# Kernel tuning notes

Measured on AMD Instinct MI355X. Metric: run time of the kernel, lower is better.

The kernel has to match this reference:

```python
import jax, jax.numpy as jnp
import numpy as np

NMS_THRESH = 0.5
SCORE_THRESH = 0.05
MAX_DET = 300


def _iou_one_vs_all(box, boxes):
    # box: [4] (x1,y1,x2,y2); boxes: [N,4]
    x1 = jnp.maximum(box[0], boxes[:, 0])
    y1 = jnp.maximum(box[1], boxes[:, 1])
    x2 = jnp.minimum(box[2], boxes[:, 2])
    y2 = jnp.minimum(box[3], boxes[:, 3])
    inter = jnp.maximum(x2 - x1, 0.0) * jnp.maximum(y2 - y1, 0.0)
    area_a = (box[2] - box[0]) * (box[3] - box[1])
    area_b = (boxes[:, 2] - boxes[:, 0]) * (boxes[:, 3] - boxes[:, 1])
    union = area_a + area_b - inter
    return inter / jnp.maximum(union, 1e-8)


def _nms_single_class(boxes, scores):
    # Greedy NMS with max_output_size=MAX_DET, matching tf.image.non_max_suppression
    # after score-threshold prefiltering. boxes:[N,4], scores:[N].
    s0 = jnp.where(scores > SCORE_THRESH, scores, -jnp.inf)

    def step(s, _):
        i = jnp.argmax(s)
        si = s[i]
        sel = jnp.isfinite(si)  # False once no candidates remain
        iou = _iou_one_vs_all(boxes[i], boxes)
        s = jnp.where(sel & (iou > NMS_THRESH), -jnp.inf, s)
        s = s.at[i].set(-jnp.inf)
        return s, (i, si, sel)

    _, (idx, sv, sel) = jax.lax.scan(step, s0, None, length=MAX_DET)
    # unselected slots carry -inf score
    return idx.astype(jnp.int32), jnp.where(sel, sv, -jnp.inf)


def _filter_one_image(boxes, classification, other):
    # boxes:[N,4], classification:[N,C], other:[N,D]
    C = classification.shape[1]
    # class-specific NMS (class_specific_filter=True, nms=True)
    idx, sv = jax.vmap(lambda c: _nms_single_class(boxes, classification[:, c]))(
        jnp.arange(C))  # each [C, MAX_DET]
    labels = jnp.broadcast_to(jnp.arange(C)[:, None], idx.shape)
    cand_scores = sv.reshape(-1)          # [C*MAX_DET]
    cand_idx = idx.reshape(-1)
    cand_lab = labels.reshape(-1)
    # global top-k over all per-class survivors
    top_s, top_i = jax.lax.top_k(cand_scores, MAX_DET)
    sel_idx = cand_idx[top_i]
    sel_lab = cand_lab[top_i]
    valid = jnp.isfinite(top_s)
    # pad invalid slots with -1 (matches tf.pad(..., constant_values=-1))
    out_boxes = jnp.where(valid[:, None], boxes[sel_idx], -1.0)
    out_scores = jnp.where(valid, top_s, -1.0)
    out_labels = jnp.where(valid, sel_lab, -1).astype(jnp.int32)
    out_other = jnp.where(valid[:, None], other[sel_idx], -1.0)
    return out_boxes, out_scores, out_labels, out_other


def setup_inputs() -> dict:
    key = jax.random.key(0)
    k1, k2, k3, k4 = jax.random.split(key, 4)
    B, N, C, D = 16, 50000, 8, 2
    xy = jax.random.uniform(k1, (B, N, 2), jnp.float32, 0.0, 512.0)
    wh = jax.random.uniform(k2, (B, N, 2), jnp.float32, 4.0, 100.0)
    boxes = jnp.concatenate([xy, xy + wh], axis=-1)  # valid (x1,y1,x2,y2)
    classification = jax.random.uniform(k3, (B, N, C), jnp.float32)
    other = jax.random.normal(k4, (B, N, D), jnp.float32)
    return {"boxes": boxes, "classification": classification, "other": other}


def reference(boxes, classification, other):
    # tf.map_fn over batch -> vmap over batch
    return jax.vmap(_filter_one_image)(boxes, classification, other)
```

## Files before the change

### kernel.cpp

```cpp
#include <hip/hip_runtime.h>
#include <math.h>
#include <stdint.h>

#define NB 16
#define NN 50000
#define NC 8
#define ND 2
#define MAX_DET 300
#define NMS_T 0.5f
#define SCORE_T 0.05f
#define CAP 1024
#define CUTBIN 252
#define LBUF 128
#define NTILE32 32
#define CHUNK 128
#define NT 512
#define NPI (NN * NC)
#define F4PB (NPI / 4 / NTILE32)

typedef unsigned long long u64;

__device__ __forceinline__ float neg_inf() { return -__builtin_inff(); }

__device__ __forceinline__ bool iou_gt(float ax1, float ay1, float ax2, float ay2,
                                       float area_a,
                                       float bx1, float by1, float bx2, float by2) {
    float x1 = fmaxf(ax1, bx1), y1 = fmaxf(ay1, by1);
    float x2 = fminf(ax2, bx2), y2 = fminf(ay2, by2);
    float inter = __fmul_rn(fmaxf(__fsub_rn(x2, x1), 0.0f),
                            fmaxf(__fsub_rn(y2, y1), 0.0f));
    float area_b = __fmul_rn(__fsub_rn(bx2, bx1), __fsub_rn(by2, by1));
    float uni = __fsub_rn(__fadd_rn(area_a, area_b), inter);
    return inter > __fmul_rn(0.5f, fmaxf(uni, 1e-8f));
}

__device__ __forceinline__ u64 score_key(float s, int n) {
    unsigned u = __float_as_uint(s);
    u ^= (u & 0x80000000u) ? 0xFFFFFFFFu : 0x80000000u;
    return ((u64)u << 32) | (unsigned)(~(unsigned)n);
}

__device__ __forceinline__ u64 shfl_xor_u64(u64 v, int m) {
    unsigned lo = (unsigned)v, hi = (unsigned)(v >> 32);
    lo = __shfl_xor(lo, m, 64);
    hi = __shfl_xor(hi, m, 64);
    return ((u64)hi << 32) | lo;
}

__global__ __launch_bounds__(1024) void compact_kernel(
    const float* __restrict__ cls, int* __restrict__ tcnt_g,
    u64* __restrict__ cand)
{
    const int b = blockIdx.x >> 5, t32 = blockIdx.x & 31;
    const int tid = threadIdx.x;
    __shared__ u64 buf[8][LBUF];
    __shared__ int lcnt[8];
    if (tid < 8) lcnt[tid] = 0;
    __syncthreads();

    const float4* c4 = (const float4*)(cls + (size_t)b * NPI);
    const int f0 = t32 * F4PB, fend = f0 + F4PB;

    for (int f = f0 + tid; f < fend; f += 1024) {
        float4 v = c4[f];
        int cb = (f & 1) * 4;
        int n = f >> 1;
        float vv[4] = {v.x, v.y, v.z, v.w};
        #pragma unroll
        for (int k = 0; k < 4; ++k) {
            float s = vv[k];
            if (s > SCORE_T) {
                int bn = (int)(s * 256.0f); if (bn > 255) bn = 255;
                if (bn >= CUTBIN) {
                    int c = cb + k;
                    int pos = atomicAdd(&lcnt[c], 1);
                    if (pos < LBUF) buf[c][pos] = score_key(s, n);
                }
            }
        }
    }
    __syncthreads();
    {
        int c = tid >> 7, i = tid & (LBUF - 1);
        int m = lcnt[c];
        if (i < (m < LBUF ? m : LBUF))
            cand[(size_t)(((b * 8 + c) * NTILE32) + t32) * LBUF + i] = buf[c][i];
        if (i == 0) tcnt_g[(b * 8 + c) * NTILE32 + t32] = m;
    }
}

__global__ __launch_bounds__(NT) void nms_fused(
    const float* __restrict__ boxes, const float* __restrict__ cls,
    const u64* __restrict__ cand, const int* __restrict__ tcnt_g,
    int* __restrict__ sel_idx, float* __restrict__ sel_score)
{
    const int bc = blockIdx.x;
    const int b = bc >> 3, c = bc & 7;
    const int tid = threadIdx.x;
    const int lane = tid & 63, widx = tid >> 6;
    const float4* bx4 = (const float4*)(boxes + (size_t)b * NN * 4);
    const float* sr = cls + (size_t)b * NN * NC + c;
    int* si = sel_idx + bc * MAX_DET;
    float* ss = sel_score + bc * MAX_DET;

    __shared__ u64 keys[CAP];
    __shared__ int tcnt_s[NTILE32], toff_s[NTILE32];
    __shared__ int sh_total, sh_ovf;
    __shared__ float4 cbox2[2][CHUNK];
    __shared__ float  carea2[2][CHUNK];
    __shared__ int    cidx2[2][CHUNK];
    __shared__ float  cscore2[2][CHUNK];
    __shared__ unsigned M32[4][CHUNK];
    __shared__ unsigned presup4[4][CHUNK];
    __shared__ u64 accmask_s[2];
    __shared__ float4 abox[MAX_DET];
    __shared__ float aarea[MAX_DET];
    __shared__ unsigned bm[(NN + 31) / 32];
    __shared__ float rv[NT];
    __shared__ int   ri[NT];
    __shared__ float sboxsh[5];

    if (tid < 64) {
        int v = (lane < NTILE32) ? tcnt_g[bc * NTILE32 + lane] : 0;
        int incl = v;
        #pragma unroll
        for (int d = 1; d < 32; d <<= 1) {
            int o = __shfl_up(incl, d, 64);
            if (lane >= d) incl += o;
        }
        if (lane < NTILE32) { tcnt_s[lane] = v; toff_s[lane] = incl - v; }
        u64 ov = __ballot(lane < NTILE32 && v > LBUF);
        if (lane == 31) { sh_total = incl; sh_ovf = (ov != 0); }
    }
    __syncthreads();
    const int cnt = sh_total;
    const bool full_fb = sh_ovf || (cnt > CAP);
    const int inSet = cnt < CAP ? cnt : CAP;

    int n_acc = 0;
    if (!full_fb) {
        for (int i = tid; i < CAP; i += NT) keys[i] = 0ull;
        __syncthreads();
        for (int s = tid; s < NTILE32 * LBUF; s += NT) {
            int t = s >> 7, i = s & (LBUF - 1);
            if (i < tcnt_s[t])
                keys[toff_s[t] + i] = cand[(size_t)(bc * NTILE32 + t) * LBUF + i];
        }
        __syncthreads();

        const int p0 = widx * 128 + lane, p1 = p0 + 64;
        u64 v0 = keys[p0];
        u64 v1 = keys[p1];
        #pragma unroll
        for (int k = 2; k <= 128; k <<= 1) {
            #pragma unroll
            for (int j = k >> 1; j > 0; j >>= 1) {
                if (j == 64) {
                    bool dir = ((p0 & k) == 0);
                    if ((v0 < v1) == dir) { u64 t = v0; v0 = v1; v1 = t; }
                } else {
                    bool lower = ((lane & j) == 0);
                    bool dir0 = ((p0 & k) == 0);
                    bool dir1 = ((p1 & k) == 0);
                    u64 o0 = shfl_xor_u64(v0, j);
                    u64 mx0 = v0 > o0 ? v0 : o0, mn0 = v0 > o0 ? o0 : v0;
                    v0 = (lower == dir0) ? mx0 : mn0;
                    u64 o1 = shfl_xor_u64(v1, j);
                    u64 mx1 = v1 > o1 ? v1 : o1, mn1 = v1 > o1 ? o1 : v1;
                    v1 = (lower == dir1) ? mx1 : mn1;
                }
            }
        }
        __syncthreads();
        for (int k = 256; k <= CAP; k <<= 1) {
            keys[p0] = v0; keys[p1] = v1;
            __syncthreads();
            for (int j = k >> 1; j >= 128; j >>= 1) {
                int p = tid;
                int i = 2 * p - (p & (j - 1));
                int ix = i + j;
                bool dir = ((i & k) == 0);
                u64 a = keys[i], b2 = keys[ix];
                if ((a < b2) == dir) { keys[i] = b2; keys[ix] = a; }
                __syncthreads();
            }
            v0 = keys[p0]; v1 = keys[p1];
            {
                bool dir = ((p0 & k) == 0);
                if ((v0 < v1) == dir) { u64 t = v0; v0 = v1; v1 = t; }
            }
            #pragma unroll
            for (int j = 32; j > 0; j >>= 1) {
                bool lower = ((lane & j) == 0);
                bool dir = ((p0 & k) == 0);
                u64 o0 = shfl_xor_u64(v0, j);
                u64 mx0 = v0 > o0 ? v0 : o0, mn0 = v0 > o0 ? o0 : v0;
                v0 = (lower == dir) ? mx0 : mn0;
                u64 o1 = shfl_xor_u64(v1, j);
                u64 mx1 = v1 > o1 ? v1 : o1, mn1 = v1 > o1 ? o1 : v1;
                v1 = (lower == dir) ? mx1 : mn1;
            }
            __syncthreads();
        }
        keys[p0] = v0; keys[p1] = v1;
        __syncthreads();

        if (tid < CHUNK && tid < inSet) {
            u64 key = keys[tid];
            int idx = (int)(~(unsigned)key);
            unsigned u = (unsigned)(key >> 32);
            unsigned uo = (u & 0x80000000u) ? (u ^ 0x80000000u) : (~u);
            float4 bb = bx4[idx];
            cbox2[0][tid] = bb;
            carea2[0][tid] = __fmul_rn(__fsub_rn(bb.z, bb.x), __fsub_rn(bb.w, bb.y));
            cidx2[0][tid] = idx; cscore2[0][tid] = __uint_as_float(uo);
        }
        __syncthreads();

        int base = 0, cur = 0;
        while (n_acc < MAX_DET && base < inSet) {
            int m = inSet - base; if (m > CHUNK) m = CHUNK;

            {
                int i = tid & (CHUNK - 1);
                int q = tid >> 7;
                if (i < m) {
                    float4 B = cbox2[cur][i];
                    unsigned p = 0;
                    int t = q;
                    for (; t + 12 < n_acc; t += 16) {
                        float4 A0 = abox[t];      float r0 = aarea[t];
                        float4 A1 = abox[t + 4];  float r1 = aarea[t + 4];
                        float4 A2 = abox[t + 8];  float r2 = aarea[t + 8];
                        float4 A3 = abox[t + 12]; float r3 = aarea[t + 12];
                        bool s0 = iou_gt(A0.x,A0.y,A0.z,A0.w,r0,B.x,B.y,B.z,B.w);
                        bool s1 = iou_gt(A1.x,A1.y,A1.z,A1.w,r1,B.x,B.y,B.z,B.w);
                        bool s2 = iou_gt(A2.x,A2.y,A2.z,A2.w,r2,B.x,B.y,B.z,B.w);
                        bool s3 = iou_gt(A3.x,A3.y,A3.z,A3.w,r3,B.x,B.y,B.z,B.w);
                        if (s0 || s1 || s2 || s3) { p = 1; break; }
                    }
                    if (!p) {
                        for (; t < n_acc; t += 4) {
                            float4 A = abox[t];
                            if (iou_gt(A.x,A.y,A.z,A.w,aarea[t],
                                       B.x,B.y,B.z,B.w)) { p = 1; break; }
                        }
                    }
                    presup4[q][i] = p;
                    unsigned bits = 0;
                    int j0 = q * 32;
                    int jend = i - j0; if (jend > 32) jend = 32;
                    int jj = 0;
                    for (; jj + 3 < jend; jj += 4) {
                        int j = j0 + jj;
                        float4 A0 = cbox2[cur][j];     float r0 = carea2[cur][j];
                        float4 A1 = cbox2[cur][j + 1]; float r1 = carea2[cur][j + 1];
                        float4 A2 = cbox2[cur][j + 2]; float r2 = carea2[cur][j + 2];
                        float4 A3 = cbox2[cur][j + 3]; float r3 = carea2[cur][j + 3];
                        if (iou_gt(A0.x,A0.y,A0.z,A0.w,r0,B.x,B.y,B.z,B.w)) bits |= 1u << jj;
                        if (iou_gt(A1.x,A1.y,A1.z,A1.w,r1,B.x,B.y,B.z,B.w)) bits |= 1u << (jj+1);
                        if (iou_gt(A2.x,A2.y,A2.z,A2.w,r2,B.x,B.y,B.z,B.w)) bits |= 1u << (jj+2);
                        if (iou_gt(A3.x,A3.y,A3.z,A3.w,r3,B.x,B.y,B.z,B.w)) bits |= 1u << (jj+3);
                    }
                    for (; jj < jend; ++jj) {
                        int j = j0 + jj;
                        float4 A = cbox2[cur][j];
                        if (iou_gt(A.x,A.y,A.z,A.w,carea2[cur][j],
                                   B.x,B.y,B.z,B.w)) bits |= 1u << jj;
                    }
                    M32[q][i] = bits;
                }
            }
            __syncthreads();

            int nbase = base + m;
            if (tid < 64) {
                u64 a0 = 0, a1 = 0;
                int ngroups = (m + 63) >> 6;
                for (int gg = 0; gg < ngroups; ++gg) {
                    int i = gg * 64 + lane;
                    unsigned pe = 1; u64 mg = 0;
                    if (i < m) {
                        pe = presup4[0][i] | presup4[1][i] | presup4[2][i] | presup4[3][i];
                        mg = (u64)M32[2 * gg][i] | ((u64)M32[2 * gg + 1][i] << 32);
                        if (gg > 0) {
                            u64 w0 = (u64)M32[0][i] | ((u64)M32[1][i] << 32);
                            if (w0 & a0) pe = 1;
                        }
                    }
                    u64 rem = ~__ballot(pe != 0);
                    u64 accw = 0;
                    while (rem) {
                        int l = __builtin_ctzll(rem);
                        accw |= 1ull << l;
                        rem &= ~(1ull << l);
                        u64 supm = __ballot(((mg >> l) & 1ull) != 0);
                        rem &= ~supm;
                    }
                    if (gg == 0) a0 = accw; else a1 = accw;
                }
                if (lane == 0) { accmask_s[0] = a0; accmask_s[1] = a1; }
            } else if (nbase < inSet) {
                int w = tid - 64;
                if (w < CHUNK && nbase + w < inSet) {
                    u64 key = keys[nbase + w];
                    int idx = (int)(~(unsigned)key);
                    unsigned u = (unsigned)(key >> 32);
                    unsigned uo = (u & 0x80000000u) ? (u ^ 0x80000000u) : (~u);
                    float4 bb = bx4[idx];
                    cbox2[cur ^ 1][w] = bb;
                    carea2[cur ^ 1][w] = __fmul_rn(__fsub_rn(bb.z, bb.x), __fsub_rn(bb.w, bb.y));
                    cidx2[cur ^ 1][w] = idx; cscore2[cur ^ 1][w] = __uint_as_float(uo);
                }
            }
            __syncthreads();

            u64 a0 = accmask_s[0], a1 = accmask_s[1];
            int add = __popcll(a0) + __popcll(a1);
            if (tid < m) {
                int gg = tid >> 6, o = tid & 63;
                u64 aw = (gg == 0) ? a0 : a1;
                if ((aw >> o) & 1ull) {
                    int rank = (gg > 0) ? __popcll(a0) : 0;
                    rank += __popcll(aw & ((1ull << o) - 1ull));
                    int pos = n_acc + rank;
                    if (pos < MAX_DET) {
                        abox[pos] = cbox2[cur][tid]; aarea[pos] = carea2[cur][tid];
                        si[pos] = cidx2[cur][tid]; ss[pos] = cscore2[cur][tid];
                    }
                }
            }
            n_acc += add; if (n_acc > MAX_DET) n_acc = MAX_DET;
            base = nbase; cur ^= 1;
            __syncthreads();
        }
    }

    const bool part_fb = (!full_fb) && (n_acc < MAX_DET);

    if (full_fb || part_fb) {
        const int BMW = (NN + 31) / 32;
        for (int i = tid; i < BMW; i += NT) bm[i] = 0u;
        __syncthreads();
        if (full_fb) {
            n_acc = 0;
        } else {
            for (int n = tid; n < NN; n += NT) {
                float4 bbn = bx4[n];
                int s = 0;
                for (int t = 0; t < n_acc; ++t) {
                    float4 A = abox[t];
                    if (iou_gt(A.x, A.y, A.z, A.w, aarea[t],
                               bbn.x, bbn.y, bbn.z, bbn.w)) s = 1;
                }
                if (s) atomicOr(&bm[n >> 5], 1u << (n & 31));
            }
        }
        __syncthreads();

        for (int k = n_acc; k < MAX_DET; ++k) {
            float bv = neg_inf(); int bi = 0x7fffffff;
            for (int n = tid; n < NN; n += NT) {
                if (!((bm[n >> 5] >> (n & 31)) & 1u)) {
                    float v = sr[(size_t)n * NC];
                    if (v > SCORE_T && v > bv) { bv = v; bi = n; }
                }
            }
            rv[tid] = bv; ri[tid] = bi;
            __syncthreads();
            for (int s = NT / 2; s > 0; s >>= 1) {
                if (tid < s) {
                    float ov = rv[tid + s]; int oi = ri[tid + s];
                    if (ov > rv[tid] || (ov == rv[tid] && oi < ri[tid])) { rv[tid] = ov; ri[tid] = oi; }
                }
                __syncthreads();
            }
            float mval = rv[0]; int midx = ri[0];
            if (mval == neg_inf()) {
                for (int kk = k + tid; kk < MAX_DET; kk += NT) { si[kk] = 0; ss[kk] = neg_inf(); }
                break;
            }
            if (tid == 0) {
                si[k] = midx; ss[k] = mval;
                float4 sb = bx4[midx];
                sboxsh[0] = sb.x; sboxsh[1] = sb.y; sboxsh[2] = sb.z; sboxsh[3] = sb.w;
                sboxsh[4] = __fmul_rn(__fsub_rn(sb.z, sb.x), __fsub_rn(sb.w, sb.y));
            }
            __syncthreads();
            float ax1 = sboxsh[0], ay1 = sboxsh[1], ax2 = sboxsh[2], ay2 = sboxsh[3];
            float area_a = sboxsh[4];
            for (int n = tid; n < NN; n += NT) {
                float4 bbn = bx4[n];
                if (iou_gt(ax1, ay1, ax2, ay2, area_a,
                           bbn.x, bbn.y, bbn.z, bbn.w))
                    atomicOr(&bm[n >> 5], 1u << (n & 31));
            }
            __syncthreads();
        }
    } else {
        for (int kk = n_acc + tid; kk < MAX_DET; kk += NT) { si[kk] = 0; ss[kk] = neg_inf(); }
    }
}

__global__ __launch_bounds__(1024) void topk_kernel(
    const float* __restrict__ boxes, const float* __restrict__ other,
    const int* __restrict__ sel_idx, const float* __restrict__ sel_score,
    float* __restrict__ out)
{
    const int b = blockIdx.x;
    const int tid = threadIdx.x;
    __shared__ u64 keys[4096];

    for (int i = tid; i < 4096; i += 1024) {
        int c = i >> 9, o = i & 511;
        u64 key = 0ull;
        if (o < MAX_DET) {
            int m = c * MAX_DET + o;
            float v = sel_score[b * NC * MAX_DET + m];
            unsigned u = __float_as_uint(v);
            u ^= (u & 0x80000000u) ? 0xFFFFFFFFu : 0x80000000u;
            key = ((u64)u << 32) | (unsigned)(~(unsigned)m);
        }
        keys[i] = key;
    }

    for (int seg = 1024; seg <= 4096; seg <<= 1) {
        int half = seg >> 1;
        __syncthreads();
        {
            int p = tid;
            int s = p / (half >> 1), t = p % (half >> 1);
            int i0 = s * seg + half + t;
            int i1 = s * seg + seg - 1 - t;
            u64 a = keys[i0]; keys[i0] = keys[i1]; keys[i1] = a;
        }
        __syncthreads();
        for (int j = half; j > 0; j >>= 1) {
            for (int p = tid; p < 2048; p += 1024) {
                int i = 2 * p - (p & (j - 1));
                int ix = i + j;
                u64 a = keys[i], bq = keys[ix];
                if (a < bq) { keys[i] = bq; keys[ix] = a; }
            }
            if (j >= 128) __syncthreads(); else __threadfence_block();
        }
    }
    __syncthreads();

    const float4* bx4 = (const float4*)(boxes + (size_t)b * NN * 4);
    const float*  ot  = other + (size_t)b * NN * ND;
    float* ob = out;
    float* os = out + NB * MAX_DET * 4;
    float* ol = os + NB * MAX_DET;
    float* oo = ol + NB * MAX_DET;

    for (int k = tid; k < MAX_DET; k += 1024) {
        u64 key = keys[k];
        unsigned u = (unsigned)(key >> 32);
        unsigned uo = (u & 0x80000000u) ? (u ^ 0x80000000u) : (u ^ 0xFFFFFFFFu);
        float score = __uint_as_float(uo);
        bool valid = isfinite(score);
        float b0=-1.f,b1=-1.f,b2=-1.f,b3=-1.f,scv=-1.f,lab=-1.f,o0=-1.f,o1=-1.f;
        if (valid) {
            int m = (int)(~(unsigned)key);
            int c = m / MAX_DET, slot = m - c * MAX_DET;
            int n = sel_idx[(b * NC + c) * MAX_DET + slot];
            float4 bb = bx4[n];
            b0 = bb.x; b1 = bb.y; b2 = bb.z; b3 = bb.w;
            scv = score; lab = (float)c;
            o0 = ot[n * ND + 0]; o1 = ot[n * ND + 1];
        }
        int base = b * MAX_DET + k;
        ob[base * 4 + 0] = b0; ob[base * 4 + 1] = b1;
        ob[base * 4 + 2] = b2; ob[base * 4 + 3] = b3;
        os[base] = scv; ol[base] = lab;
        oo[base * 2 + 0] = o0; oo[base * 2 + 1] = o1;
    }
}

extern "C" void kernel_launch(void* const* d_in, const int* in_sizes, int n_in,
                              void* d_out, int out_size, void* d_ws, size_t ws_size,
                              hipStream_t stream) {
    const float* boxes = (const float*)d_in[0];
    const float* cls   = (const float*)d_in[1];
    const float* other = (const float*)d_in[2];
    float* out = (float*)d_out;

    int* tcnt_g = (int*)d_ws;
    u64* cand  = (u64*)(tcnt_g + NB * NC * NTILE32);
    int* sel_idx = (int*)(cand + (size_t)NB * NC * NTILE32 * LBUF);
    float* sel_score = (float*)(sel_idx + NB * NC * MAX_DET);

    compact_kernel<<<NB * NTILE32, 1024, 0, stream>>>(cls, tcnt_g, cand);
    nms_fused<<<NB * NC, NT, 0, stream>>>(boxes, cls, cand, tcnt_g,
                                          sel_idx, sel_score);
    topk_kernel<<<NB, 1024, 0, stream>>>(boxes, other, sel_idx, sel_score, out);
}
```

Measured before the change: 67.16 us.

## Widen NMS chunk to 256 with 1024 threads and fixed-point acceptance resolve

Doubles the candidate chunk processed per iteration to 256 and the block to 1024 threads. Within-chunk suppression masks are stored as 64-bit words. The serial ctz-driven greedy acceptance loop over 64-lane groups is replaced by a ballot-based fixed-point iteration across all four groups at once. The candidate box area is also precomputed once and passed into the IoU test. The aim is fewer chunk iterations and less serial resolve latency, at the cost of a bitonic sort that leaves half the threads idle, more shared memory and register pressure, and a possibly long fixed-point loop.

```diff
diff --git a/kernel.cpp b/kernel.cpp
--- a/kernel.cpp
+++ b/kernel.cpp
@@ -13,8 +13,8 @@
 #define CUTBIN 252
 #define LBUF 128
 #define NTILE32 32
-#define CHUNK 128
-#define NT 512
+#define CHUNK 256
+#define NT 1024
 #define NPI (NN * NC)
 #define F4PB (NPI / 4 / NTILE32)
 
@@ -24,12 +24,12 @@
 
 __device__ __forceinline__ bool iou_gt(float ax1, float ay1, float ax2, float ay2,
                                        float area_a,
-                                       float bx1, float by1, float bx2, float by2) {
+                                       float bx1, float by1, float bx2, float by2,
+                                       float area_b) {
     float x1 = fmaxf(ax1, bx1), y1 = fmaxf(ay1, by1);
     float x2 = fminf(ax2, bx2), y2 = fminf(ay2, by2);
     float inter = __fmul_rn(fmaxf(__fsub_rn(x2, x1), 0.0f),
                             fmaxf(__fsub_rn(y2, y1), 0.0f));
-    float area_b = __fmul_rn(__fsub_rn(bx2, bx1), __fsub_rn(by2, by1));
     float uni = __fsub_rn(__fadd_rn(area_a, area_b), inter);
     return inter > __fmul_rn(0.5f, fmaxf(uni, 1e-8f));
 }
@@ -97,7 +97,7 @@
     const int bc = blockIdx.x;
     const int b = bc >> 3, c = bc & 7;
     const int tid = threadIdx.x;
-    const int lane = tid & 63, widx = tid >> 6;
+    const int lane = tid & 63;
     const float4* bx4 = (const float4*)(boxes + (size_t)b * NN * 4);
     const float* sr = cls + (size_t)b * NN * NC + c;
     int* si = sel_idx + bc * MAX_DET;
@@ -106,13 +106,13 @@
     __shared__ u64 keys[CAP];
     __shared__ int tcnt_s[NTILE32], toff_s[NTILE32];
     __shared__ int sh_total, sh_ovf;
+    __shared__ u64 M64[4][CHUNK];
+    __shared__ unsigned presup4[4][CHUNK];
     __shared__ float4 cbox2[2][CHUNK];
     __shared__ float  carea2[2][CHUNK];
     __shared__ int    cidx2[2][CHUNK];
     __shared__ float  cscore2[2][CHUNK];
-    __shared__ unsigned M32[4][CHUNK];
-    __shared__ unsigned presup4[4][CHUNK];
-    __shared__ u64 accmask_s[2];
+    __shared__ u64 accs4_s[4];
     __shared__ float4 abox[MAX_DET];
     __shared__ float aarea[MAX_DET];
     __shared__ unsigned bm[(NN + 31) / 32];
@@ -148,61 +148,67 @@
         }
         __syncthreads();
 
-        const int p0 = widx * 128 + lane, p1 = p0 + 64;
-        u64 v0 = keys[p0];
-        u64 v1 = keys[p1];
-        #pragma unroll
-        for (int k = 2; k <= 128; k <<= 1) {
+        const int p0 = (tid >> 6) * 128 + lane, p1 = p0 + 64;
+        u64 v0 = 0, v1 = 0;
+        if (tid < 512) {
+            v0 = keys[p0]; v1 = keys[p1];
             #pragma unroll
-            for (int j = k >> 1; j > 0; j >>= 1) {
-                if (j == 64) {
+            for (int k = 2; k <= 128; k <<= 1) {
+                #pragma unroll
+                for (int j = k >> 1; j > 0; j >>= 1) {
+                    if (j == 64) {
+                        bool dir = ((p0 & k) == 0);
+                        if ((v0 < v1) == dir) { u64 t = v0; v0 = v1; v1 = t; }
+                    } else {
+                        bool lower = ((lane & j) == 0);
+                        bool dir0 = ((p0 & k) == 0);
+                        bool dir1 = ((p1 & k) == 0);
+                        u64 o0 = shfl_xor_u64(v0, j);
+                        u64 mx0 = v0 > o0 ? v0 : o0, mn0 = v0 > o0 ? o0 : v0;
+                        v0 = (lower == dir0) ? mx0 : mn0;
+                        u64 o1 = shfl_xor_u64(v1, j);
+                        u64 mx1 = v1 > o1 ? v1 : o1, mn1 = v1 > o1 ? o1 : v1;
+                        v1 = (lower == dir1) ? mx1 : mn1;
+                    }
+                }
+            }
+        }
+        __syncthreads();
+        for (int k = 256; k <= CAP; k <<= 1) {
+            if (tid < 512) { keys[p0] = v0; keys[p1] = v1; }
+            __syncthreads();
+            for (int j = k >> 1; j >= 128; j >>= 1) {
+                if (tid < 512) {
+                    int p = tid;
+                    int i = 2 * p - (p & (j - 1));
+                    int ix = i + j;
+                    bool dir = ((i & k) == 0);
+                    u64 a = keys[i], b2 = keys[ix];
+                    if ((a < b2) == dir) { keys[i] = b2; keys[ix] = a; }
+                }
+                __syncthreads();
+            }
+            if (tid < 512) {
+                v0 = keys[p0]; v1 = keys[p1];
+                {
                     bool dir = ((p0 & k) == 0);
                     if ((v0 < v1) == dir) { u64 t = v0; v0 = v1; v1 = t; }
-                } else {
+                }
+                #pragma unroll
+                for (int j = 32; j > 0; j >>= 1) {
                     bool lower = ((lane & j) == 0);
-                    bool dir0 = ((p0 & k) == 0);
-                    bool dir1 = ((p1 & k) == 0);
+                    bool dir = ((p0 & k) == 0);
                     u64 o0 = shfl_xor_u64(v0, j);
                     u64 mx0 = v0 > o0 ? v0 : o0, mn0 = v0 > o0 ? o0 : v0;
-                    v0 = (lower == dir0) ? mx0 : mn0;
+                    v0 = (lower == dir) ? mx0 : mn0;
                     u64 o1 = shfl_xor_u64(v1, j);
                     u64 mx1 = v1 > o1 ? v1 : o1, mn1 = v1 > o1 ? o1 : v1;
-                    v1 = (lower == dir1) ? mx1 : mn1;
-                }
-            }
-        }
-        __syncthreads();
-        for (int k = 256; k <= CAP; k <<= 1) {
-            keys[p0] = v0; keys[p1] = v1;
-            __syncthreads();
-            for (int j = k >> 1; j >= 128; j >>= 1) {
-                int p = tid;
-                int i = 2 * p - (p & (j - 1));
-                int ix = i + j;
-                bool dir = ((i & k) == 0);
-                u64 a = keys[i], b2 = keys[ix];
-                if ((a < b2) == dir) { keys[i] = b2; keys[ix] = a; }
-                __syncthreads();
-            }
-            v0 = keys[p0]; v1 = keys[p1];
-            {
-                bool dir = ((p0 & k) == 0);
-                if ((v0 < v1) == dir) { u64 t = v0; v0 = v1; v1 = t; }
-            }
-            #pragma unroll
-            for (int j = 32; j > 0; j >>= 1) {
-                bool lower = ((lane & j) == 0);
-                bool dir = ((p0 & k) == 0);
-                u64 o0 = shfl_xor_u64(v0, j);
-                u64 mx0 = v0 > o0 ? v0 : o0, mn0 = v0 > o0 ? o0 : v0;
-                v0 = (lower == dir) ? mx0 : mn0;
-                u64 o1 = shfl_xor_u64(v1, j);
-                u64 mx1 = v1 > o1 ? v1 : o1, mn1 = v1 > o1 ? o1 : v1;
-                v1 = (lower == dir) ? mx1 : mn1;
-            }
-            __syncthreads();
-        }
-        keys[p0] = v0; keys[p1] = v1;
+                    v1 = (lower == dir) ? mx1 : mn1;
+                }
+            }
+            __syncthreads();
+        }
+        if (tid < 512) { keys[p0] = v0; keys[p1] = v1; }
         __syncthreads();
 
         if (tid < CHUNK && tid < inSet) {
@@ -223,86 +229,112 @@
 
             {
                 int i = tid & (CHUNK - 1);
-                int q = tid >> 7;
+                int q = tid >> 8;
                 if (i < m) {
                     float4 B = cbox2[cur][i];
+                    float  Barea = carea2[cur][i];
                     unsigned p = 0;
                     int t = q;
-                    for (; t + 12 < n_acc; t += 16) {
+                    for (; t + 28 < n_acc; t += 32) {
                         float4 A0 = abox[t];      float r0 = aarea[t];
                         float4 A1 = abox[t + 4];  float r1 = aarea[t + 4];
                         float4 A2 = abox[t + 8];  float r2 = aarea[t + 8];
                         float4 A3 = abox[t + 12]; float r3 = aarea[t + 12];
-                        bool s0 = iou_gt(A0.x,A0.y,A0.z,A0.w,r0,B.x,B.y,B.z,B.w);
-                        bool s1 = iou_gt(A1.x,A1.y,A1.z,A1.w,r1,B.x,B.y,B.z,B.w);
-                        bool s2 = iou_gt(A2.x,A2.y,A2.z,A2.w,r2,B.x,B.y,B.z,B.w);
-                        bool s3 = iou_gt(A3.x,A3.y,A3.z,A3.w,r3,B.x,B.y,B.z,B.w);
-                        if (s0 || s1 || s2 || s3) { p = 1; break; }
+                        float4 A4 = abox[t + 16]; float r4 = aarea[t + 16];
+                        float4 A5 = abox[t + 20]; float r5 = aarea[t + 20];
+                        float4 A6 = abox[t + 24]; float r6 = aarea[t + 24];
+                        float4 A7 = abox[t + 28]; float r7 = aarea[t + 28];
+                        bool s0 = iou_gt(A0.x,A0.y,A0.z,A0.w,r0,B.x,B.y,B.z,B.w,Barea);
+                        bool s1 = iou_gt(A1.x,A1.y,A1.z,A1.w,r1,B.x,B.y,B.z,B.w,Barea);
+                        bool s2 = iou_gt(A2.x,A2.y,A2.z,A2.w,r2,B.x,B.y,B.z,B.w,Barea);
+                        bool s3 = iou_gt(A3.x,A3.y,A3.z,A3.w,r3,B.x,B.y,B.z,B.w,Barea);
+                        bool s4 = iou_gt(A4.x,A4.y,A4.z,A4.w,r4,B.x,B.y,B.z,B.w,Barea);
+                        bool s5 = iou_gt(A5.x,A5.y,A5.z,A5.w,r5,B.x,B.y,B.z,B.w,Barea);
+                        bool s6 = iou_gt(A6.x,A6.y,A6.z,A6.w,r6,B.x,B.y,B.z,B.w,Barea);
+                        bool s7 = iou_gt(A7.x,A7.y,A7.z,A7.w,r7,B.x,B.y,B.z,B.w,Barea);
+                        if (s0|s1|s2|s3|s4|s5|s6|s7) { p = 1; break; }
                     }
                     if (!p) {
                         for (; t < n_acc; t += 4) {
                             float4 A = abox[t];
                             if (iou_gt(A.x,A.y,A.z,A.w,aarea[t],
-                                       B.x,B.y,B.z,B.w)) { p = 1; break; }
+                                       B.x,B.y,B.z,B.w,Barea)) { p = 1; break; }
                         }
                     }
                     presup4[q][i] = p;
-                    unsigned bits = 0;
-                    int j0 = q * 32;
-                    int jend = i - j0; if (jend > 32) jend = 32;
+                    u64 bits = 0;
+                    int j0 = q * 64;
+                    int jend = i - j0; if (jend > 64) jend = 64; if (jend < 0) jend = 0;
                     int jj = 0;
-                    for (; jj + 3 < jend; jj += 4) {
+                    for (; jj + 7 < jend; jj += 8) {
                         int j = j0 + jj;
                         float4 A0 = cbox2[cur][j];     float r0 = carea2[cur][j];
                         float4 A1 = cbox2[cur][j + 1]; float r1 = carea2[cur][j + 1];
                         float4 A2 = cbox2[cur][j + 2]; float r2 = carea2[cur][j + 2];
                         float4 A3 = cbox2[cur][j + 3]; float r3 = carea2[cur][j + 3];
-                        if (iou_gt(A0.x,A0.y,A0.z,A0.w,r0,B.x,B.y,B.z,B.w)) bits |= 1u << jj;
-                        if (iou_gt(A1.x,A1.y,A1.z,A1.w,r1,B.x,B.y,B.z,B.w)) bits |= 1u << (jj+1);
-                        if (iou_gt(A2.x,A2.y,A2.z,A2.w,r2,B.x,B.y,B.z,B.w)) bits |= 1u << (jj+2);
-                        if (iou_gt(A3.x,A3.y,A3.z,A3.w,r3,B.x,B.y,B.z,B.w)) bits |= 1u << (jj+3);
+                        float4 A4 = cbox2[cur][j + 4]; float r4 = carea2[cur][j + 4];
+                        float4 A5 = cbox2[cur][j + 5]; float r5 = carea2[cur][j + 5];
+                        float4 A6 = cbox2[cur][j + 6]; float r6 = carea2[cur][j + 6];
+                        float4 A7 = cbox2[cur][j + 7]; float r7 = carea2[cur][j + 7];
+                        if (iou_gt(A0.x,A0.y,A0.z,A0.w,r0,B.x,B.y,B.z,B.w,Barea)) bits |= 1ull << jj;
+                        if (iou_gt(A1.x,A1.y,A1.z,A1.w,r1,B.x,B.y,B.z,B.w,Barea)) bits |= 1ull << (jj+1);
+                        if (iou_gt(A2.x,A2.y,A2.z,A2.w,r2,B.x,B.y,B.z,B.w,Barea)) bits |= 1ull << (jj+2);
+                        if (iou_gt(A3.x,A3.y,A3.z,A3.w,r3,B.x,B.y,B.z,B.w,Barea)) bits |= 1ull << (jj+3);
+                        if (iou_gt(A4.x,A4.y,A4.z,A4.w,r4,B.x,B.y,B.z,B.w,Barea)) bits |= 1ull << (jj+4);
+                        if (iou_gt(A5.x,A5.y,A5.z,A5.w,r5,B.x,B.y,B.z,B.w,Barea)) bits |= 1ull << (jj+5);
+                        if (iou_gt(A6.x,A6.y,A6.z,A6.w,r6,B.x,B.y,B.z,B.w,Barea)) bits |= 1ull << (jj+6);
+                        if (iou_gt(A7.x,A7.y,A7.z,A7.w,r7,B.x,B.y,B.z,B.w,Barea)) bits |= 1ull << (jj+7);
                     }
                     for (; jj < jend; ++jj) {
                         int j = j0 + jj;
                         float4 A = cbox2[cur][j];
                         if (iou_gt(A.x,A.y,A.z,A.w,carea2[cur][j],
-                                   B.x,B.y,B.z,B.w)) bits |= 1u << jj;
-                    }
-                    M32[q][i] = bits;
+                                   B.x,B.y,B.z,B.w,Barea)) bits |= 1ull << jj;
+                    }
+                    M64[q][i] = bits;
                 }
             }
             __syncthreads();
 
             int nbase = base + m;
             if (tid < 64) {
-                u64 a0 = 0, a1 = 0;
-                int ngroups = (m + 63) >> 6;
-                for (int gg = 0; gg < ngroups; ++gg) {
-                    int i = gg * 64 + lane;
-                    unsigned pe = 1; u64 mg = 0;
+                u64 Mr[4][4];
+                unsigned pe[4];
+                bool acc[4];
+                #pragma unroll
+                for (int cg = 0; cg < 4; ++cg) {
+                    int i = cg * 64 + lane;
                     if (i < m) {
-                        pe = presup4[0][i] | presup4[1][i] | presup4[2][i] | presup4[3][i];
-                        mg = (u64)M32[2 * gg][i] | ((u64)M32[2 * gg + 1][i] << 32);
-                        if (gg > 0) {
-                            u64 w0 = (u64)M32[0][i] | ((u64)M32[1][i] << 32);
-                            if (w0 & a0) pe = 1;
-                        }
-                    }
-                    u64 rem = ~__ballot(pe != 0);
-                    u64 accw = 0;
-                    while (rem) {
-                        int l = __builtin_ctzll(rem);
-                        accw |= 1ull << l;
-                        rem &= ~(1ull << l);
-                        u64 supm = __ballot(((mg >> l) & 1ull) != 0);
-                        rem &= ~supm;
-                    }
-                    if (gg == 0) a0 = accw; else a1 = accw;
-                }
-                if (lane == 0) { accmask_s[0] = a0; accmask_s[1] = a1; }
-            } else if (nbase < inSet) {
-                int w = tid - 64;
-                if (w < CHUNK && nbase + w < inSet) {
+                        pe[cg] = presup4[0][i] | presup4[1][i] | presup4[2][i] | presup4[3][i];
+                        #pragma unroll
+                        for (int w = 0; w < 4; ++w) Mr[cg][w] = M64[w][i];
+                    } else {
+                        pe[cg] = 1u;
+                        #pragma unroll
+                        for (int w = 0; w < 4; ++w) Mr[cg][w] = 0ull;
+                    }
+                    acc[cg] = (pe[cg] == 0);
+                }
+                u64 a0 = __ballot(acc[0]), a1 = __ballot(acc[1]);
+                u64 a2 = __ballot(acc[2]), a3 = __ballot(acc[3]);
+                for (int it = 0; it < CHUNK + 1; ++it) {
+                    #pragma unroll
+                    for (int cg = 0; cg < 4; ++cg) {
+                        u64 sup = (Mr[cg][0] & a0) | (Mr[cg][1] & a1)
+                                | (Mr[cg][2] & a2) | (Mr[cg][3] & a3);
+                        acc[cg] = (pe[cg] == 0) && (sup == 0ull);
+                    }
+                    u64 n0 = __ballot(acc[0]), n1 = __ballot(acc[1]);
+                    u64 n2 = __ballot(acc[2]), n3 = __ballot(acc[3]);
+                    bool same = (n0 == a0) && (n1 == a1) && (n2 == a2) && (n3 == a3);
+                    a0 = n0; a1 = n1; a2 = n2; a3 = n3;
+                    if (same) break;
+                }
+                if (lane == 0) { accs4_s[0] = a0; accs4_s[1] = a1;
+                                 accs4_s[2] = a2; accs4_s[3] = a3; }
+            } else if (tid >= 256 && tid < 512 && nbase < inSet) {
+                int w = tid - 256;
+                if (nbase + w < inSet) {
                     u64 key = keys[nbase + w];
                     int idx = (int)(~(unsigned)key);
                     unsigned u = (unsigned)(key >> 32);
@@ -315,13 +347,16 @@
             }
             __syncthreads();
 
-            u64 a0 = accmask_s[0], a1 = accmask_s[1];
-            int add = __popcll(a0) + __popcll(a1);
+            u64 a0 = accs4_s[0], a1 = accs4_s[1], a2 = accs4_s[2], a3 = accs4_s[3];
+            int add = __popcll(a0) + __popcll(a1) + __popcll(a2) + __popcll(a3);
             if (tid < m) {
                 int gg = tid >> 6, o = tid & 63;
-                u64 aw = (gg == 0) ? a0 : a1;
+                u64 aw = (gg == 0) ? a0 : (gg == 1) ? a1 : (gg == 2) ? a2 : a3;
                 if ((aw >> o) & 1ull) {
-                    int rank = (gg > 0) ? __popcll(a0) : 0;
+                    int rank = 0;
+                    if (gg > 0) rank += __popcll(a0);
+                    if (gg > 1) rank += __popcll(a1);
+                    if (gg > 2) rank += __popcll(a2);
                     rank += __popcll(aw & ((1ull << o) - 1ull));
                     int pos = n_acc + rank;
                     if (pos < MAX_DET) {
@@ -347,11 +382,12 @@
         } else {
             for (int n = tid; n < NN; n += NT) {
                 float4 bbn = bx4[n];
+                float nb_area = __fmul_rn(__fsub_rn(bbn.z, bbn.x), __fsub_rn(bbn.w, bbn.y));
                 int s = 0;
                 for (int t = 0; t < n_acc; ++t) {
                     float4 A = abox[t];
                     if (iou_gt(A.x, A.y, A.z, A.w, aarea[t],
-                               bbn.x, bbn.y, bbn.z, bbn.w)) s = 1;
+                               bbn.x, bbn.y, bbn.z, bbn.w, nb_area)) s = 1;
                 }
                 if (s) atomicOr(&bm[n >> 5], 1u << (n & 31));
             }
@@ -391,8 +427,9 @@
             float area_a = sboxsh[4];
             for (int n = tid; n < NN; n += NT) {
                 float4 bbn = bx4[n];
+                float nb_area = __fmul_rn(__fsub_rn(bbn.z, bbn.x), __fsub_rn(bbn.w, bbn.y));
                 if (iou_gt(ax1, ay1, ax2, ay2, area_a,
-                           bbn.x, bbn.y, bbn.z, bbn.w))
+                           bbn.x, bbn.y, bbn.z, bbn.w, nb_area))
                     atomicOr(&bm[n >> 5], 1u << (n & 31));
             }
             __syncthreads();
```

Measured after the change: 64.36 us (median of 2 runs). -4.2%, faster.
